# Kernel tuning notes

Hardware: AMD Instinct MI355X
Metric: run time of the kernel (lower is better)

The kernel has to match this reference:

```python
import jax, jax.numpy as jnp
import numpy as np

VOCAB = 4  # token alphabet size used in setup_inputs


def setup_inputs() -> dict:
    key = jax.random.key(0)
    k1, k2 = jax.random.split(key)
    xq = jax.random.randint(k1, (8192, 512), 0, VOCAB, dtype=jnp.int32)
    xp = jax.random.randint(k2, (8192, 512), 0, VOCAB, dtype=jnp.int32)
    return {"xq": xq, "xp": xp}


def reference(xq, xp):
    # Pairwise Hamming distance: dists[n, m] = sum_d [xq[n, d] != xp[m, d]].
    # Expressed as D minus the match count, computed as a one-hot GEMM
    # (matches[n,m] = sum_{d,v} 1[xq[n,d]==v] * 1[xp[m,d]==v]) so the whole
    # NxMxD reduction is a single fused contraction instead of the original
    # per-row broadcast-compare loop. Exact in fp32 since counts <= D = 512.
    D = xq.shape[1]
    qh = jax.nn.one_hot(xq, VOCAB, dtype=jnp.float32)  # [N, D, V]
    ph = jax.nn.one_hot(xp, VOCAB, dtype=jnp.float32)  # [M, D, V]
    matches = jnp.einsum('ndv,mdv->nm', qh, ph)        # [N, M]
    return (jnp.float32(D) - matches).astype(jnp.int32)
```

## Files before the change

### kernel.cpp

```cpp
#include <hip/hip_runtime.h>
#include <stdint.h>


#define NROWS  8192
#define NTOK   512
#define KB     1536
#define BM     128
#define BK     64
#define KSTEPS (KB / BK)
#define NTHREADS 256

typedef int v4i __attribute__((ext_vector_type(4)));

__global__ __launch_bounds__(256) void pack_kernel(
    const int* __restrict__ xq, const int* __restrict__ xp,
    uint32_t* __restrict__ qpk, uint32_t* __restrict__ ppk) {
  int idx = blockIdx.x * 256 + threadIdx.x;
  int row = idx >> 7, q = idx & 127;

  const int4 a = ((const int4*)xq)[(size_t)row * 128 + q];
  const int4 b = ((const int4*)xp)[(size_t)row * 128 + q];
  int ta[4] = {a.x, a.y, a.z, a.w};
  int tb[4] = {b.x, b.y, b.z, b.w};

  uint32_t qa0 = 0, qa1 = 0, qa2 = 0, pb0 = 0, pb1 = 0, pb2 = 0;
  #pragma unroll
  for (int j = 0; j < 4; ++j) {
    int b1 = (ta[j] >> 1) & 1, b0 = ta[j] & 1;
    qa0 |= ((uint32_t)(uint8_t)(1 - 2 * b1)) << (8 * j);
    qa1 |= ((uint32_t)(uint8_t)(1 - 2 * b0)) << (8 * j);
    qa2 |= ((uint32_t)(uint8_t)(1 - 2 * (b1 ^ b0))) << (8 * j);
    b1 = (tb[j] >> 1) & 1; b0 = tb[j] & 1;
    pb0 |= ((uint32_t)(uint8_t)(1 - 2 * b1)) << (8 * j);
    pb1 |= ((uint32_t)(uint8_t)(1 - 2 * b0)) << (8 * j);
    pb2 |= ((uint32_t)(uint8_t)(1 - 2 * (b1 ^ b0))) << (8 * j);
  }
  size_t base = (size_t)row * 384 + q;
  qpk[base]       = qa0;  ppk[base]       = pb0;
  qpk[base + 128] = qa1;  ppk[base + 128] = pb1;
  qpk[base + 256] = qa2;  ppk[base + 256] = pb2;
}

__global__ __launch_bounds__(NTHREADS) void hamming_mfma(
    const uint8_t* __restrict__ Q, const uint8_t* __restrict__ P,
    int* __restrict__ out) {
  __shared__ __align__(1024) uint8_t As[BM * BK];
  __shared__ __align__(1024) uint8_t Bs[BM * BK];

  const int t = threadIdx.x;
  const int l = t & 63;
  const int w = t >> 6;
  const int wr = w >> 1, wc = w & 1;
  const int br = blockIdx.y, bc = blockIdx.x;

  const uint8_t* qbase = Q + (size_t)br * BM * KB;
  const uint8_t* pbase = P + (size_t)bc * BM * KB;

  const int srow0 = w * 32 + (l >> 2);
  const int sseg  = ((l & 3) ^ ((l >> 3) & 3)) * 16;

  v4i acc[4][4] = {};

  for (int kk = 0; kk < KSTEPS; ++kk) {
    const int kb = kk * BK;
    #pragma unroll
    for (int i = 0; i < 2; ++i) {
      const int s = w * 2 + i;
      const int row = srow0 + i * 16;
      const uint8_t* ga = qbase + (size_t)row * KB + kb + sseg;
      const uint8_t* gb = pbase + (size_t)row * KB + kb + sseg;
      __builtin_amdgcn_global_load_lds(
          (const __attribute__((address_space(1))) void*)ga,
          (__attribute__((address_space(3))) void*)(As + s * 1024), 16, 0, 0);
      __builtin_amdgcn_global_load_lds(
          (const __attribute__((address_space(1))) void*)gb,
          (__attribute__((address_space(3))) void*)(Bs + s * 1024), 16, 0, 0);
    }
    __syncthreads();

    v4i af[4], bf[4];
    #pragma unroll
    for (int m = 0; m < 4; ++m) {
      const int row = wr * 64 + m * 16 + (l & 15);
      const int seg = ((l >> 4) ^ ((row >> 1) & 3)) * 16;
      af[m] = *(const v4i*)(As + row * BK + seg);
    }
    #pragma unroll
    for (int n = 0; n < 4; ++n) {
      const int row = wc * 64 + n * 16 + (l & 15);
      const int seg = ((l >> 4) ^ ((row >> 1) & 3)) * 16;
      bf[n] = *(const v4i*)(Bs + row * BK + seg);
    }

    #pragma unroll
    for (int m = 0; m < 4; ++m)
      #pragma unroll
      for (int n = 0; n < 4; ++n)
        acc[m][n] = __builtin_amdgcn_mfma_i32_16x16x64_i8(af[m], bf[n], acc[m][n], 0, 0, 0);

    __syncthreads();
  }

  const int row0 = br * BM + wr * 64 + (l >> 4) * 4;
  const int col0 = bc * BM + wc * 64 + (l & 15);
  #pragma unroll
  for (int m = 0; m < 4; ++m)
    #pragma unroll
    for (int n = 0; n < 4; ++n) {
      const size_t rbase = (size_t)(row0 + m * 16) * NROWS + (col0 + n * 16);
      #pragma unroll
      for (int r = 0; r < 4; ++r)
        out[rbase + (size_t)r * NROWS] = NTOK - ((acc[m][n][r] + 512) >> 2);
    }
}

extern "C" void kernel_launch(void* const* d_in, const int* in_sizes, int n_in,
                              void* d_out, int out_size, void* d_ws, size_t ws_size,
                              hipStream_t stream) {
  const int* xq = (const int*)d_in[0];
  const int* xp = (const int*)d_in[1];
  int* out = (int*)d_out;

  uint32_t* qpk = (uint32_t*)d_ws;
  uint32_t* ppk = qpk + (size_t)NROWS * KB / 4;

  pack_kernel<<<(NROWS * 128) / 256, 256, 0, stream>>>(xq, xp, qpk, ppk);

  dim3 grid(NROWS / BM, NROWS / BM);
  hamming_mfma<<<grid, NTHREADS, 0, stream>>>((const uint8_t*)qpk,
                                              (const uint8_t*)ppk, out);
}
```

Measured before the change: 386.6 us.

## Rewrite Hamming GEMM with 256x256 tiles, 32x32 MFMA, double-buffered LDS and pre-tiled packing

The pack kernel now writes the ±1 int8 operands in a pre-tiled layout that matches the MFMA fragment order, so the GEMM can stream whole tiles into LDS with contiguous global_load_lds transfers. The GEMM kernel moves from 128x128 tiles with 256 threads to 256x256 tiles with 512 threads, and from 16x16x64 to 32x32x32 int8 MFMA. It double-buffers 128KB of LDS with fine-grained vmcnt waits, barriers, setprio and a blockIdx swizzle for L2 locality. The aim is more operand reuse, overlap of loads with compute, and fewer LDS bank conflicts. The cost is one block per CU because of the large LDS footprint, and heavier register pressure.

```diff
diff --git a/kernel.cpp b/kernel.cpp
--- a/kernel.cpp
+++ b/kernel.cpp
@@ -2,115 +2,143 @@
 #include <stdint.h>
 
 
-#define NROWS  8192
-#define NTOK   512
-#define KB     1536
-#define BM     128
-#define BK     64
-#define KSTEPS (KB / BK)
-#define NTHREADS 256
+#define NROWS 8192
+#define NTOK  512
+#define KBYT  1536
+#define BM    256
+#define KT    12
+#define THREADS 512
 
-typedef int v4i __attribute__((ext_vector_type(4)));
+typedef int v4i  __attribute__((ext_vector_type(4)));
+typedef int v16i __attribute__((ext_vector_type(16)));
+
+#define AS1(p) ((const __attribute__((address_space(1))) void*)(p))
+#define AS3(p) ((__attribute__((address_space(3))) void*)(p))
 
 __global__ __launch_bounds__(256) void pack_kernel(
     const int* __restrict__ xq, const int* __restrict__ xp,
-    uint32_t* __restrict__ qpk, uint32_t* __restrict__ ppk) {
-  int idx = blockIdx.x * 256 + threadIdx.x;
-  int row = idx >> 7, q = idx & 127;
+    uint8_t* __restrict__ qpk, uint8_t* __restrict__ ppk) {
+  const int bid = blockIdx.x;
+  const int sg  = bid & 7;
+  const int rest = bid >> 3;
+  const int kt  = rest % 12;
+  const int R   = rest / 12;
+  const int r   = threadIdx.x;
 
-  const int4 a = ((const int4*)xq)[(size_t)row * 128 + q];
-  const int4 b = ((const int4*)xp)[(size_t)row * 128 + q];
-  int ta[4] = {a.x, a.y, a.z, a.w};
-  int tb[4] = {b.x, b.y, b.z, b.w};
+  const int kb0 = kt * 128 + sg * 16;
+  const int c   = kb0 >> 9;
+  const int d0  = kb0 & 511;
+  const int row = R * 256 + r;
 
-  uint32_t qa0 = 0, qa1 = 0, qa2 = 0, pb0 = 0, pb1 = 0, pb2 = 0;
+  const int4* qv = (const int4*)(xq + (size_t)row * NTOK + d0);
+  const int4* pv = (const int4*)(xp + (size_t)row * NTOK + d0);
+
+  uint32_t qw[4], pw[4];
   #pragma unroll
-  for (int j = 0; j < 4; ++j) {
-    int b1 = (ta[j] >> 1) & 1, b0 = ta[j] & 1;
-    qa0 |= ((uint32_t)(uint8_t)(1 - 2 * b1)) << (8 * j);
-    qa1 |= ((uint32_t)(uint8_t)(1 - 2 * b0)) << (8 * j);
-    qa2 |= ((uint32_t)(uint8_t)(1 - 2 * (b1 ^ b0))) << (8 * j);
-    b1 = (tb[j] >> 1) & 1; b0 = tb[j] & 1;
-    pb0 |= ((uint32_t)(uint8_t)(1 - 2 * b1)) << (8 * j);
-    pb1 |= ((uint32_t)(uint8_t)(1 - 2 * b0)) << (8 * j);
-    pb2 |= ((uint32_t)(uint8_t)(1 - 2 * (b1 ^ b0))) << (8 * j);
+  for (int i = 0; i < 4; ++i) {
+    int4 a = qv[i], b = pv[i];
+    int ta[4] = {a.x, a.y, a.z, a.w};
+    int tb[4] = {b.x, b.y, b.z, b.w};
+    uint32_t wq = 0, wp = 0;
+    #pragma unroll
+    for (int j = 0; j < 4; ++j) {
+      int bq = (c == 0) ? ((ta[j] >> 1) & 1) : (c == 1) ? (ta[j] & 1)
+                        : (((ta[j] >> 1) ^ ta[j]) & 1);
+      int bp = (c == 0) ? ((tb[j] >> 1) & 1) : (c == 1) ? (tb[j] & 1)
+                        : (((tb[j] >> 1) ^ tb[j]) & 1);
+      wq |= (uint32_t)((uint8_t)(1 - 2 * bq)) << (8 * j);
+      wp |= (uint32_t)((uint8_t)(1 - 2 * bp)) << (8 * j);
+    }
+    qw[i] = wq; pw[i] = wp;
   }
-  size_t base = (size_t)row * 384 + q;
-  qpk[base]       = qa0;  ppk[base]       = pb0;
-  qpk[base + 128] = qa1;  ppk[base + 128] = pb1;
-  qpk[base + 256] = qa2;  ppk[base + 256] = pb2;
+  const size_t off = ((size_t)bid * 256 + r) * 16;
+  *(uint4*)(qpk + off) = make_uint4(qw[0], qw[1], qw[2], qw[3]);
+  *(uint4*)(ppk + off) = make_uint4(pw[0], pw[1], pw[2], pw[3]);
 }
 
-__global__ __launch_bounds__(NTHREADS) void hamming_mfma(
-    const uint8_t* __restrict__ Q, const uint8_t* __restrict__ P,
+__global__ __launch_bounds__(THREADS) void hamming_mfma(
+    const uint8_t* __restrict__ Apk, const uint8_t* __restrict__ Bpk,
     int* __restrict__ out) {
-  __shared__ __align__(1024) uint8_t As[BM * BK];
-  __shared__ __align__(1024) uint8_t Bs[BM * BK];
+  __shared__ __align__(128) uint8_t lds[131072];
 
   const int t = threadIdx.x;
   const int l = t & 63;
   const int w = t >> 6;
-  const int wr = w >> 1, wc = w & 1;
-  const int br = blockIdx.y, bc = blockIdx.x;
+  const int wr = w >> 2, wc = w & 3;
 
-  const uint8_t* qbase = Q + (size_t)br * BM * KB;
-  const uint8_t* pbase = P + (size_t)bc * BM * KB;
+  const int bid = blockIdx.x;
+  const int nid = (bid & 7) * 128 + (bid >> 3);
+  const int br = nid >> 5, bc = nid & 31;
 
-  const int srow0 = w * 32 + (l >> 2);
-  const int sseg  = ((l & 3) ^ ((l >> 3) & 3)) * 16;
+  const uint8_t* Abase = Apk + (size_t)br * (KT * 4 * 8192);
+  const uint8_t* Bbase = Bpk + (size_t)bc * (KT * 4 * 8192);
 
-  v4i acc[4][4] = {};
+  const int stoff = w * 1024 + l * 16;
+  const int g4   = (l >> 5) * 4096;
+  const int arow = (l & 31) * 16;
 
-  for (int kk = 0; kk < KSTEPS; ++kk) {
-    const int kb = kk * BK;
-    #pragma unroll
-    for (int i = 0; i < 2; ++i) {
-      const int s = w * 2 + i;
-      const int row = srow0 + i * 16;
-      const uint8_t* ga = qbase + (size_t)row * KB + kb + sseg;
-      const uint8_t* gb = pbase + (size_t)row * KB + kb + sseg;
-      __builtin_amdgcn_global_load_lds(
-          (const __attribute__((address_space(1))) void*)ga,
-          (__attribute__((address_space(3))) void*)(As + s * 1024), 16, 0, 0);
-      __builtin_amdgcn_global_load_lds(
-          (const __attribute__((address_space(1))) void*)gb,
-          (__attribute__((address_space(3))) void*)(Bs + s * 1024), 16, 0, 0);
-    }
-    __syncthreads();
+  v16i acc[4][2] = {};
 
-    v4i af[4], bf[4];
-    #pragma unroll
-    for (int m = 0; m < 4; ++m) {
-      const int row = wr * 64 + m * 16 + (l & 15);
-      const int seg = ((l >> 4) ^ ((row >> 1) & 3)) * 16;
-      af[m] = *(const v4i*)(As + row * BK + seg);
-    }
-    #pragma unroll
-    for (int n = 0; n < 4; ++n) {
-      const int row = wc * 64 + n * 16 + (l & 15);
-      const int seg = ((l >> 4) ^ ((row >> 1) & 3)) * 16;
-      bf[n] = *(const v4i*)(Bs + row * BK + seg);
-    }
+  #pragma unroll
+  for (int p = 0; p < 4; ++p) {
+    __builtin_amdgcn_global_load_lds(AS1(Abase + p * 8192 + stoff),
+                                     AS3(lds + p * 8192 + stoff), 16, 0, 0);
+    __builtin_amdgcn_global_load_lds(AS1(Bbase + p * 8192 + stoff),
+                                     AS3(lds + 32768 + p * 8192 + stoff), 16, 0, 0);
+  }
+
+  for (int kk = 0; kk < KT; ++kk) {
+    const int cur = kk & 1;
+    const int ktn = (kk + 1 == KT) ? 0 : kk + 1;
+    const uint8_t* an = Abase + (size_t)ktn * (4 * 8192);
+    const uint8_t* bn = Bbase + (size_t)ktn * (4 * 8192);
+    uint8_t* ldsc = lds + cur * 65536;
+    uint8_t* ldsn = lds + (cur ^ 1) * 65536;
 
     #pragma unroll
-    for (int m = 0; m < 4; ++m)
+    for (int p = 0; p < 4; ++p) {
+      asm volatile("s_waitcnt vmcnt(6)" ::: "memory");
+      __builtin_amdgcn_s_barrier();
+      __builtin_amdgcn_global_load_lds(AS1(an + p * 8192 + stoff),
+                                       AS3(ldsn + p * 8192 + stoff), 16, 0, 0);
+      __builtin_amdgcn_global_load_lds(AS1(bn + p * 8192 + stoff),
+                                       AS3(ldsn + 32768 + p * 8192 + stoff), 16, 0, 0);
+      const uint8_t* ab = ldsc + p * 8192 + g4;
+      const uint8_t* bb = ldsc + 32768 + p * 8192 + g4;
+      v4i af[4], bf[2];
       #pragma unroll
-      for (int n = 0; n < 4; ++n)
-        acc[m][n] = __builtin_amdgcn_mfma_i32_16x16x64_i8(af[m], bf[n], acc[m][n], 0, 0, 0);
+      for (int m = 0; m < 4; ++m)
+        af[m] = *(const v4i*)(ab + (wr * 128 + m * 32) * 16 + arow);
+      #pragma unroll
+      for (int n = 0; n < 2; ++n)
+        bf[n] = *(const v4i*)(bb + (wc * 64 + n * 32) * 16 + arow);
+      asm volatile("s_waitcnt lgkmcnt(0)" ::: "memory");
+      __builtin_amdgcn_sched_barrier(0);
+      __builtin_amdgcn_s_setprio(1);
+      #pragma unroll
+      for (int m = 0; m < 4; ++m)
+        #pragma unroll
+        for (int n = 0; n < 2; ++n)
+          acc[m][n] = __builtin_amdgcn_mfma_i32_32x32x32_i8(af[m], bf[n],
+                                                            acc[m][n], 0, 0, 0);
+      __builtin_amdgcn_s_setprio(0);
+      __builtin_amdgcn_s_barrier();
+    }
+  }
+  asm volatile("s_waitcnt vmcnt(0)" ::: "memory");
 
-    __syncthreads();
-  }
-
-  const int row0 = br * BM + wr * 64 + (l >> 4) * 4;
-  const int col0 = bc * BM + wc * 64 + (l & 15);
+  const int rbase = br * BM + wr * 128 + 4 * (l >> 5);
+  const int cbase = bc * BM + wc * 64 + (l & 31);
   #pragma unroll
   for (int m = 0; m < 4; ++m)
     #pragma unroll
-    for (int n = 0; n < 4; ++n) {
-      const size_t rbase = (size_t)(row0 + m * 16) * NROWS + (col0 + n * 16);
+    for (int n = 0; n < 2; ++n) {
+      const int col = cbase + n * 32;
       #pragma unroll
-      for (int r = 0; r < 4; ++r)
-        out[rbase + (size_t)r * NROWS] = NTOK - ((acc[m][n][r] + 512) >> 2);
+      for (int reg = 0; reg < 16; ++reg) {
+        const int orow = rbase + m * 32 + (reg & 3) + 8 * (reg >> 2);
+        out[(size_t)orow * NROWS + col] = NTOK - ((acc[m][n][reg] + 512) >> 2);
+      }
     }
 }
 
@@ -121,12 +149,9 @@
   const int* xp = (const int*)d_in[1];
   int* out = (int*)d_out;
 
-  uint32_t* qpk = (uint32_t*)d_ws;
-  uint32_t* ppk = qpk + (size_t)NROWS * KB / 4;
+  uint8_t* qpk = (uint8_t*)d_ws;
+  uint8_t* ppk = qpk + (size_t)NROWS * KBYT;
 
-  pack_kernel<<<(NROWS * 128) / 256, 256, 0, stream>>>(xq, xp, qpk, ppk);
-
-  dim3 grid(NROWS / BM, NROWS / BM);
-  hamming_mfma<<<grid, NTHREADS, 0, stream>>>((const uint8_t*)qpk,
-                                              (const uint8_t*)ppk, out);
+  pack_kernel<<<3072, 256, 0, stream>>>(xq, xp, qpk, ppk);
+  hamming_mfma<<<1024, THREADS, 0, stream>>>(qpk, ppk, out);
 }
```

Result: no change. 392.0 us (+1.4%).
